# Optimization experiments

Measured on AMD Instinct MI355X. Metric: run time of the kernel, lower is better.

## Reference

```python
import jax, jax.numpy as jnp
import numpy as np

NUM_CLASS = 32
ALPHA = 1.0
GAMMA = 2.0
EPS = 1e-8  # torch F.cosine_similarity norm clamp


def setup_inputs() -> dict:
    key = jax.random.key(0)
    k1, k2 = jax.random.split(key)
    B, D, W, H, C = 8, 256, 160, 160, NUM_CLASS
    decod_feature = jax.random.normal(k1, (B, D, W, H), dtype=jnp.float32)
    mask = (jax.random.uniform(k2, (B, C, W, H)) < 0.05).astype(jnp.float32)
    return {"decod_feature": decod_feature, "mask": mask}


def reference(decod_feature, mask):
    # Per class c: gather feature vectors f_i (dim D) at pixels where mask==1,
    # sum cosine_similarity(f_i, f_j) over i<j, divide by n(n+1)/2.
    # With unit-normalized u_i: sum_{i<j} u_i.u_j = (||sum_i u_i||^2 - n) / 2.
    norms = jnp.sqrt(jnp.sum(decod_feature * decod_feature, axis=1, keepdims=True))
    U = decod_feature / jnp.maximum(norms, EPS)          # [B,D,W,H] normalized pixel features
    s = jnp.einsum('bdwh,bcwh->cd', U, mask)             # [C,D] per-class sum of unit vectors
    n = jnp.sum(mask, axis=(0, 2, 3))                    # [C] pixels per class
    pair_sum = (jnp.sum(s * s, axis=1) - n) * 0.5        # sum over i<j of cos sims
    denom = n * (n + 1.0) * 0.5
    class_loss = jnp.where(n > 0, pair_sum / jnp.maximum(denom, 1.0), 0.0)
    emb_loss = jnp.sum(class_loss) / NUM_CLASS
    return ALPHA * jnp.exp(-GAMMA * emb_loss)
```

## Files before the change

kernel.cpp:

```cpp
#include <hip/hip_runtime.h>
#include <hip/hip_bf16.h>
#include <cstdint>
#include <cstddef>

#define NUM_CLASS 32
#define D_DIM 256
#define PIX_PER_IMG 25600
#define TILE_PX 64
#define TILES_PER_IMG 400
#define N_TILES 3200
#define BLOCK_THREADS 512
#define MAX_GRID 256

typedef __attribute__((ext_vector_type(4))) float  f32x4;
typedef __attribute__((ext_vector_type(8))) __bf16 bf16x8;
typedef unsigned short ushort8 __attribute__((ext_vector_type(8)));
typedef unsigned int   uint2v  __attribute__((ext_vector_type(2)));

__device__ __forceinline__ unsigned short f2bf(float x) {
    unsigned u = __builtin_bit_cast(unsigned, x);
    unsigned r = (u + 0x7fffu + ((u >> 16) & 1u)) >> 16;
    return (unsigned short)r;
}

__device__ __forceinline__ unsigned cvt_pk_bf16(float lo, float hi) {
    unsigned r;
    asm("v_cvt_pk_bf16_f32 %0, %1, %2" : "=v"(r) : "v"(lo), "v"(hi));
    return r;
}

__device__ __forceinline__ int bt_w(int row, int p4) {
    return row * 128 + ((((p4 >> 1) ^ (row & 7)) << 4)) + ((p4 & 1) << 3);
}
__device__ __forceinline__ int bt_r(int row, int j) {
    return row * 128 + (((j ^ (row & 7)) << 4));
}

__global__ __launch_bounds__(BLOCK_THREADS, 4)
void emb_main(const float* __restrict__ feat, const float* __restrict__ mask,
              float* __restrict__ part, float* __restrict__ npart, int G)
{
    __shared__ __align__(16) unsigned char ftb[D_DIM * 128];
    __shared__ __align__(16) unsigned char mtb[NUM_CLASS * 128];
    __shared__ __align__(16) float ssq_s[8][TILE_PX];
    __shared__ __align__(16) unsigned short inv_bf[TILE_PX];

    const int t = threadIdx.x;
    const int lane = t & 63;
    const int wave = t >> 6;
    const int blk  = blockIdx.x;
    const int lh = lane >> 4;
    const int ll = lane & 15;
    const int mc  = t >> 4;
    const int mpg = t & 15;

    const int nt = (blk < N_TILES) ? ((N_TILES - 1 - blk) / G + 1) : 0;

    f32x4 acc[2][2] = {};
    float nc = 0.f;

    f32x4 fv[8];
    f32x4 mv;

    auto issue = [&](int ti) {
        const int b  = ti / TILES_PER_IMG;
        const int p0 = (ti - b * TILES_PER_IMG) * TILE_PX;
        const float* fb = feat + (size_t)b * ((size_t)D_DIM * PIX_PER_IMG) + p0 + ll * 4;
        #pragma unroll
        for (int k = 0; k < 8; ++k) {
            const int d = wave * 4 + lh + 32 * k;
            fv[k] = *(const f32x4*)(fb + (size_t)d * PIX_PER_IMG);
        }
        mv = *(const f32x4*)(mask + (size_t)b * (NUM_CLASS * PIX_PER_IMG)
                             + (size_t)mc * PIX_PER_IMG + p0 + mpg * 4);
    };

    if (nt > 0) issue(blk);

    for (int i = 0; i < nt; ++i) {
        __builtin_amdgcn_s_barrier();
        __builtin_amdgcn_sched_barrier(0);

        f32x4 ss = {0.f, 0.f, 0.f, 0.f};
        #pragma unroll
        for (int k = 0; k < 8; ++k) {
            const int d = wave * 4 + lh + 32 * k;
            ss += fv[k] * fv[k];
            uint2v w;
            w.x = cvt_pk_bf16(fv[k].x, fv[k].y);
            w.y = cvt_pk_bf16(fv[k].z, fv[k].w);
            *(uint2v*)(ftb + bt_w(d, ll)) = w;
        }
        nc += mv.x + mv.y + mv.z + mv.w;
        {
            uint2v w;
            w.x = cvt_pk_bf16(mv.x, mv.y);
            w.y = cvt_pk_bf16(mv.z, mv.w);
            *(uint2v*)(mtb + bt_w(mc, mpg)) = w;
        }
        ss.x += __shfl_down(ss.x, 32); ss.y += __shfl_down(ss.y, 32);
        ss.z += __shfl_down(ss.z, 32); ss.w += __shfl_down(ss.w, 32);
        ss.x += __shfl_down(ss.x, 16); ss.y += __shfl_down(ss.y, 16);
        ss.z += __shfl_down(ss.z, 16); ss.w += __shfl_down(ss.w, 16);
        if (lane < 16) *(f32x4*)&ssq_s[wave][lane * 4] = ss;

        if (i + 1 < nt) issue(blk + (i + 1) * G);

        __builtin_amdgcn_sched_barrier(0);
        asm volatile("s_waitcnt lgkmcnt(0)" ::: "memory");
        __builtin_amdgcn_s_barrier();
        __builtin_amdgcn_sched_barrier(0);

        if (t < TILE_PX) {
            float tot = 0.f;
            #pragma unroll
            for (int w = 0; w < 8; ++w) tot += ssq_s[w][t];
            inv_bf[t] = f2bf(1.0f / fmaxf(sqrtf(tot), 1e-8f));
        }
        __builtin_amdgcn_sched_barrier(0);
        asm volatile("s_waitcnt lgkmcnt(0)" ::: "memory");
        __builtin_amdgcn_s_barrier();
        __builtin_amdgcn_sched_barrier(0);

        const int dbase = wave * 32;
        #pragma unroll
        for (int ks = 0; ks < 2; ++ks) {
            const int j   = ks * 4 + lh;
            const int kp0 = j * 8;
            const ushort8 iv = *(const ushort8*)((const char*)inv_bf + kp0 * 2);
            const ushort8 m0 = *(const ushort8*)(mtb + bt_r(ll,      j));
            const ushort8 m1 = *(const ushort8*)(mtb + bt_r(16 + ll, j));
            const ushort8 b0 = *(const ushort8*)(ftb + bt_r(dbase + ll,      j));
            const ushort8 b1 = *(const ushort8*)(ftb + bt_r(dbase + 16 + ll, j));
            ushort8 a0, a1;
            #pragma unroll
            for (int q = 0; q < 8; ++q) {
                a0[q] = m0[q] ? iv[q] : (unsigned short)0;
                a1[q] = m1[q] ? iv[q] : (unsigned short)0;
            }
            const bf16x8 ba0 = __builtin_bit_cast(bf16x8, a0);
            const bf16x8 ba1 = __builtin_bit_cast(bf16x8, a1);
            const bf16x8 bb0 = __builtin_bit_cast(bf16x8, b0);
            const bf16x8 bb1 = __builtin_bit_cast(bf16x8, b1);
            acc[0][0] = __builtin_amdgcn_mfma_f32_16x16x32_bf16(ba0, bb0, acc[0][0], 0, 0, 0);
            acc[0][1] = __builtin_amdgcn_mfma_f32_16x16x32_bf16(ba0, bb1, acc[0][1], 0, 0, 0);
            acc[1][0] = __builtin_amdgcn_mfma_f32_16x16x32_bf16(ba1, bb0, acc[1][0], 0, 0, 0);
            acc[1][1] = __builtin_amdgcn_mfma_f32_16x16x32_bf16(ba1, bb1, acc[1][1], 0, 0, 0);
        }
        __builtin_amdgcn_sched_barrier(0);
    }

    {
        float* myout = part + (size_t)blk * (NUM_CLASS * D_DIM);
        const int dbase = wave * 32;
        #pragma unroll
        for (int m = 0; m < 2; ++m)
            #pragma unroll
            for (int n = 0; n < 2; ++n)
                #pragma unroll
                for (int r = 0; r < 4; ++r) {
                    const int c = m * 16 + lh * 4 + r;
                    const int d = dbase + n * 16 + ll;
                    myout[c * D_DIM + d] = acc[m][n][r];
                }
    }
    nc += __shfl_down(nc, 8);
    nc += __shfl_down(nc, 4);
    nc += __shfl_down(nc, 2);
    nc += __shfl_down(nc, 1);
    if (mpg == 0) npart[(size_t)blk * NUM_CLASS + mc] = nc;
}

__global__ __launch_bounds__(1024)
void emb_reduce(const float* __restrict__ part, const float* __restrict__ npart,
                float* __restrict__ cls, int G)
{
    const int c = blockIdx.x;
    const int t = threadIdx.x;
    const int d = t & 255, gs = t >> 8;
    float s = 0.f;
    #pragma unroll 8
    for (int g = gs; g < G; g += 4)
        s += part[(size_t)g * (NUM_CLASS * D_DIM) + c * D_DIM + d];
    __shared__ float red[4][256];
    red[gs][d] = s;
    float nsum = 0.f;
    for (int g = t; g < G; g += 1024) nsum += npart[(size_t)g * NUM_CLASS + c];
    __syncthreads();
    float s2 = 0.f;
    if (t < 256) {
        const float tot = red[0][t] + red[1][t] + red[2][t] + red[3][t];
        s2 = tot * tot;
    }
    const int lane = t & 63, wave = t >> 6;
    #pragma unroll
    for (int off = 32; off > 0; off >>= 1) {
        s2   += __shfl_down(s2, off);
        nsum += __shfl_down(nsum, off);
    }
    __shared__ float rs[16], rn[16];
    if (lane == 0) { rs[wave] = s2; rn[wave] = nsum; }
    __syncthreads();
    if (t == 0) {
        float S2 = 0.f, N = 0.f;
        #pragma unroll
        for (int w = 0; w < 16; ++w) { S2 += rs[w]; N += rn[w]; }
        const float pair = 0.5f * (S2 - N);
        const float den  = 0.5f * N * (N + 1.0f);
        cls[c] = (N > 0.f) ? (pair / fmaxf(den, 1.0f)) : 0.f;
    }
}

__global__ void emb_final(const float* __restrict__ cls, float* __restrict__ out)
{
    const int t = threadIdx.x;
    float v = (t < NUM_CLASS) ? cls[t] : 0.f;
    #pragma unroll
    for (int off = 32; off > 0; off >>= 1) v += __shfl_down(v, off);
    if (t == 0) {
        const float emb = v / (float)NUM_CLASS;
        out[0] = 1.0f * expf(-2.0f * emb);
    }
}

extern "C" void kernel_launch(void* const* d_in, const int* in_sizes, int n_in,
                              void* d_out, int out_size, void* d_ws, size_t ws_size,
                              hipStream_t stream)
{
    const float* feat = (const float*)d_in[0];
    const float* mask = (const float*)d_in[1];
    float* out = (float*)d_out;

    const size_t per_blk = (size_t)(NUM_CLASS * D_DIM + NUM_CLASS) * sizeof(float);
    int G = MAX_GRID;
    size_t need = (size_t)G * per_blk + NUM_CLASS * sizeof(float);
    if (ws_size < need) {
        size_t g = (ws_size > NUM_CLASS * sizeof(float))
                       ? (ws_size - NUM_CLASS * sizeof(float)) / per_blk : 1;
        if (g < 1) g = 1;
        if (g > MAX_GRID) g = MAX_GRID;
        G = (int)g;
    }
    float* part  = (float*)d_ws;
    float* npart = part + (size_t)G * (NUM_CLASS * D_DIM);
    float* cls   = npart + (size_t)G * NUM_CLASS;

    emb_main<<<G, BLOCK_THREADS, 0, stream>>>(feat, mask, part, npart, G);
    emb_reduce<<<NUM_CLASS, 1024, 0, stream>>>(part, npart, cls, G);
    emb_final<<<1, 64, 0, stream>>>(cls, out);
}
```

Baseline: 50.20 us.

## Double-buffer LDS tiles and overlap previous tile's MFMA with current staging

Feature and mask tiles now live in two LDS buffers, so the MFMA for tile i-1 runs in the same barrier phase as the bf16 staging and norm reduction for tile i. The masked inverse-norm A operand is built once per block in LDS (abuild) instead of every wave redoing the select at MFMA time. One barrier per iteration is removed from the critical path, and the final tile is drained after the loop. The cost is roughly double the LDS per block, which may cut how many blocks fit on a CU in a kernel that is likely bandwidth-bound.

```diff
diff --git a/kernel.cpp b/kernel.cpp
--- a/kernel.cpp
+++ b/kernel.cpp
@@ -15,6 +15,7 @@
 typedef __attribute__((ext_vector_type(4))) float  f32x4;
 typedef __attribute__((ext_vector_type(8))) __bf16 bf16x8;
 typedef unsigned short ushort8 __attribute__((ext_vector_type(8)));
+typedef unsigned short us4v    __attribute__((ext_vector_type(4)));
 typedef unsigned int   uint2v  __attribute__((ext_vector_type(2)));
 
 __device__ __forceinline__ unsigned short f2bf(float x) {
@@ -40,10 +41,10 @@
 void emb_main(const float* __restrict__ feat, const float* __restrict__ mask,
               float* __restrict__ part, float* __restrict__ npart, int G)
 {
-    __shared__ __align__(16) unsigned char ftb[D_DIM * 128];
-    __shared__ __align__(16) unsigned char mtb[NUM_CLASS * 128];
+    __shared__ __align__(16) unsigned char ftb[2][D_DIM * 128];
+    __shared__ __align__(16) unsigned char mtb[2][NUM_CLASS * 128];
     __shared__ __align__(16) float ssq_s[8][TILE_PX];
-    __shared__ __align__(16) unsigned short inv_bf[TILE_PX];
+    __shared__ __align__(16) unsigned short inv_bf[2][TILE_PX];
 
     const int t = threadIdx.x;
     const int lane = t & 63;
@@ -75,69 +76,28 @@
                              + (size_t)mc * PIX_PER_IMG + p0 + mpg * 4);
     };
 
-    if (nt > 0) issue(blk);
-
-    for (int i = 0; i < nt; ++i) {
-        __builtin_amdgcn_s_barrier();
-        __builtin_amdgcn_sched_barrier(0);
-
-        f32x4 ss = {0.f, 0.f, 0.f, 0.f};
-        #pragma unroll
-        for (int k = 0; k < 8; ++k) {
-            const int d = wave * 4 + lh + 32 * k;
-            ss += fv[k] * fv[k];
-            uint2v w;
-            w.x = cvt_pk_bf16(fv[k].x, fv[k].y);
-            w.y = cvt_pk_bf16(fv[k].z, fv[k].w);
-            *(uint2v*)(ftb + bt_w(d, ll)) = w;
-        }
-        nc += mv.x + mv.y + mv.z + mv.w;
-        {
-            uint2v w;
-            w.x = cvt_pk_bf16(mv.x, mv.y);
-            w.y = cvt_pk_bf16(mv.z, mv.w);
-            *(uint2v*)(mtb + bt_w(mc, mpg)) = w;
-        }
-        ss.x += __shfl_down(ss.x, 32); ss.y += __shfl_down(ss.y, 32);
-        ss.z += __shfl_down(ss.z, 32); ss.w += __shfl_down(ss.w, 32);
-        ss.x += __shfl_down(ss.x, 16); ss.y += __shfl_down(ss.y, 16);
-        ss.z += __shfl_down(ss.z, 16); ss.w += __shfl_down(ss.w, 16);
-        if (lane < 16) *(f32x4*)&ssq_s[wave][lane * 4] = ss;
-
-        if (i + 1 < nt) issue(blk + (i + 1) * G);
-
-        __builtin_amdgcn_sched_barrier(0);
-        asm volatile("s_waitcnt lgkmcnt(0)" ::: "memory");
-        __builtin_amdgcn_s_barrier();
-        __builtin_amdgcn_sched_barrier(0);
-
-        if (t < TILE_PX) {
-            float tot = 0.f;
-            #pragma unroll
-            for (int w = 0; w < 8; ++w) tot += ssq_s[w][t];
-            inv_bf[t] = f2bf(1.0f / fmaxf(sqrtf(tot), 1e-8f));
-        }
-        __builtin_amdgcn_sched_barrier(0);
-        asm volatile("s_waitcnt lgkmcnt(0)" ::: "memory");
-        __builtin_amdgcn_s_barrier();
-        __builtin_amdgcn_sched_barrier(0);
-
+    auto abuild = [&](int b) {
+        const int row = t >> 4, p4 = t & 15;
+        unsigned char* ap = mtb[b] + bt_w(row, p4);
+        const us4v m  = *(const us4v*)ap;
+        const us4v iv = *(const us4v*)&inv_bf[b][p4 * 4];
+        us4v r;
+        #pragma unroll
+        for (int q = 0; q < 4; ++q) r[q] = m[q] ? iv[q] : (unsigned short)0;
+        *(us4v*)ap = r;
+    };
+
+    auto domfma = [&](int b) {
+        const unsigned char* fb2 = ftb[b];
+        const unsigned char* mb2 = mtb[b];
         const int dbase = wave * 32;
         #pragma unroll
         for (int ks = 0; ks < 2; ++ks) {
-            const int j   = ks * 4 + lh;
-            const int kp0 = j * 8;
-            const ushort8 iv = *(const ushort8*)((const char*)inv_bf + kp0 * 2);
-            const ushort8 m0 = *(const ushort8*)(mtb + bt_r(ll,      j));
-            const ushort8 m1 = *(const ushort8*)(mtb + bt_r(16 + ll, j));
-            const ushort8 b0 = *(const ushort8*)(ftb + bt_r(dbase + ll,      j));
-            const ushort8 b1 = *(const ushort8*)(ftb + bt_r(dbase + 16 + ll, j));
-            ushort8 a0, a1;
-            #pragma unroll
-            for (int q = 0; q < 8; ++q) {
-                a0[q] = m0[q] ? iv[q] : (unsigned short)0;
-                a1[q] = m1[q] ? iv[q] : (unsigned short)0;
-            }
+            const int j = ks * 4 + lh;
+            const ushort8 a0 = *(const ushort8*)(mb2 + bt_r(ll,      j));
+            const ushort8 a1 = *(const ushort8*)(mb2 + bt_r(16 + ll, j));
+            const ushort8 b0 = *(const ushort8*)(fb2 + bt_r(dbase + ll,      j));
+            const ushort8 b1 = *(const ushort8*)(fb2 + bt_r(dbase + 16 + ll, j));
             const bf16x8 ba0 = __builtin_bit_cast(bf16x8, a0);
             const bf16x8 ba1 = __builtin_bit_cast(bf16x8, a1);
             const bf16x8 bb0 = __builtin_bit_cast(bf16x8, b0);
@@ -147,7 +107,65 @@
             acc[1][0] = __builtin_amdgcn_mfma_f32_16x16x32_bf16(ba1, bb0, acc[1][0], 0, 0, 0);
             acc[1][1] = __builtin_amdgcn_mfma_f32_16x16x32_bf16(ba1, bb1, acc[1][1], 0, 0, 0);
         }
-        __builtin_amdgcn_sched_barrier(0);
+    };
+
+    if (nt > 0) issue(blk);
+
+    for (int i = 0; i < nt; ++i) {
+        const int b = i & 1;
+
+        f32x4 ss = {0.f, 0.f, 0.f, 0.f};
+        #pragma unroll
+        for (int k = 0; k < 8; ++k) {
+            const int d = wave * 4 + lh + 32 * k;
+            ss += fv[k] * fv[k];
+            uint2v w;
+            w.x = cvt_pk_bf16(fv[k].x, fv[k].y);
+            w.y = cvt_pk_bf16(fv[k].z, fv[k].w);
+            *(uint2v*)(ftb[b] + bt_w(d, ll)) = w;
+        }
+        nc += mv.x + mv.y + mv.z + mv.w;
+        {
+            uint2v w;
+            w.x = cvt_pk_bf16(mv.x, mv.y);
+            w.y = cvt_pk_bf16(mv.z, mv.w);
+            *(uint2v*)(mtb[b] + bt_w(mc, mpg)) = w;
+        }
+        if (i + 1 < nt) issue(blk + (i + 1) * G);
+        if (i > 0) abuild(b ^ 1);
+        ss.x += __shfl_down(ss.x, 32); ss.y += __shfl_down(ss.y, 32);
+        ss.z += __shfl_down(ss.z, 32); ss.w += __shfl_down(ss.w, 32);
+        ss.x += __shfl_down(ss.x, 16); ss.y += __shfl_down(ss.y, 16);
+        ss.z += __shfl_down(ss.z, 16); ss.w += __shfl_down(ss.w, 16);
+        if (lane < 16) *(f32x4*)&ssq_s[wave][lane * 4] = ss;
+
+        __builtin_amdgcn_sched_barrier(0);
+        asm volatile("s_waitcnt lgkmcnt(0)" ::: "memory");
+        __builtin_amdgcn_s_barrier();
+        __builtin_amdgcn_sched_barrier(0);
+
+        if (t < TILE_PX) {
+            float tot = 0.f;
+            #pragma unroll
+            for (int w = 0; w < 8; ++w) tot += ssq_s[w][t];
+            inv_bf[b][t] = f2bf(1.0f / fmaxf(sqrtf(tot), 1e-8f));
+        }
+        if (i > 0) domfma(b ^ 1);
+
+        __builtin_amdgcn_sched_barrier(0);
+        asm volatile("s_waitcnt lgkmcnt(0)" ::: "memory");
+        __builtin_amdgcn_s_barrier();
+        __builtin_amdgcn_sched_barrier(0);
+    }
+
+    if (nt > 0) {
+        const int b = (nt - 1) & 1;
+        abuild(b);
+        __builtin_amdgcn_sched_barrier(0);
+        asm volatile("s_waitcnt lgkmcnt(0)" ::: "memory");
+        __builtin_amdgcn_s_barrier();
+        __builtin_amdgcn_sched_barrier(0);
+        domfma(b);
     }
 
     {
```

After: 48.94 us. 2.5% less time.
